# Optimization experiments

Hardware: AMD Instinct MI355X
Metric: run time of the kernel (lower is better)

Reference implementation:

```python
import jax, jax.numpy as jnp
import numpy as np

HEADS = 4
NEG_SLOPE = 0.2
LN_EPS = 1e-5


def _layernorm(h, g, b):
    mu = h.mean(-1, keepdims=True)
    var = ((h - mu) ** 2).mean(-1, keepdims=True)
    return (h - mu) / jnp.sqrt(var + LN_EPS) * g + b


def _forward(x, edge_attr, vnf_context,
             w_node, b_node, w_edge_emb, b_edge_emb,
             w_eproj, b_eproj, w_vnf, b_vnf,
             attn_w1, attn_b1, attn_w2, attn_b2, attn_w3, attn_b3,
             gat_w, gat_att_src, gat_att_dst, gat_we, gat_att_e, gat_b,
             ln_g, ln_b,
             venc_w1, venc_b1, venc_w2, venc_b2,
             lstm_wih, lstm_whh, lstm_bih, lstm_bhh,
             out_w1, out_b1, out_w2, out_b2, out_w3, out_b3,
             edge_index):
    N = x.shape[0]
    C = w_node.shape[1]  # hidden_dim = per-head out_channels
    L = gat_w.shape[0]
    src, dst = edge_index[0], edge_index[1]

    # embeddings
    xh = x @ w_node + b_node                        # [N, C]
    ea = edge_attr @ w_edge_emb + b_edge_emb        # [E, C]

    # EdgeAttentionLayer (vnf_context branch, no network_state)
    ef = ea @ w_eproj + b_eproj                     # [E, C]
    vemb = vnf_context @ w_vnf + b_vnf              # [C]
    comb = jnp.concatenate([ef, jnp.broadcast_to(vemb, ef.shape)], axis=-1)
    h1 = jax.nn.relu(comb @ attn_w1 + attn_b1)
    h2 = jax.nn.relu(h1 @ attn_w2 + attn_b2)
    edge_attention = jax.nn.sigmoid(h2 @ attn_w3 + attn_b3)[:, 0]   # [E]
    e_enh = ef * edge_attention[:, None]            # weighted edge features [E, C]

    # PathQualityAwareConv stack: GATConv(heads=4, concat=False, edge_dim=C)
    for l in range(L):
        xr = xh
        xs = (xh @ gat_w[l]).reshape(N, HEADS, C)               # [N, H, C]
        efeat = (e_enh @ gat_we[l]).reshape(-1, HEADS, C)        # [E, H, C]
        a = (jnp.einsum('ehc,hc->eh', xs[src], gat_att_src[l])
             + jnp.einsum('ehc,hc->eh', xs[dst], gat_att_dst[l])
             + jnp.einsum('ehc,hc->eh', efeat, gat_att_e[l]))
        a = jax.nn.leaky_relu(a, NEG_SLOPE)
        amax = jax.ops.segment_max(a, dst, num_segments=N)
        amax = jnp.where(jnp.isfinite(amax), amax, 0.0)
        ae = jnp.exp(a - amax[dst])
        denom = jax.ops.segment_sum(ae, dst, num_segments=N)
        alpha = ae / (denom[dst] + 1e-16)                        # [E, H]
        msg = xs[src] * alpha[:, :, None]                        # [E, H, C]
        agg = jax.ops.segment_sum(msg, dst, num_segments=N)      # [N, H, C]
        h = agg.mean(axis=1) + gat_b[l]                          # concat=False -> head mean
        h = _layernorm(h, ln_g[l], ln_b[l])
        xh = h + xr                                              # residual (same size)

    # vnf context encoder
    v = jax.nn.relu(vnf_context @ venc_w1 + venc_b1) @ venc_w2 + venc_b2  # [C]

    # Set2Set pooling, single graph, processing_steps=3, LSTM(2C -> C)
    hS = jnp.zeros((C,), xh.dtype)
    cS = jnp.zeros((C,), xh.dtype)
    q_star = jnp.zeros((2 * C,), xh.dtype)
    for _ in range(3):
        gates = lstm_wih @ q_star + lstm_bih + lstm_whh @ hS + lstm_bhh
        gi, gf, gg, go = jnp.split(gates, 4)
        cS = jax.nn.sigmoid(gf) * cS + jax.nn.sigmoid(gi) * jnp.tanh(gg)
        hS = jax.nn.sigmoid(go) * jnp.tanh(cS)
        q = hS
        a_sc = jax.nn.softmax(xh @ q)                            # [N]
        r = a_sc @ xh                                            # [C]
        q_star = jnp.concatenate([q, r])

    combined = jnp.concatenate([q_star, v])                      # [3C]
    o = jax.nn.relu(combined @ out_w1 + out_b1)
    o = jax.nn.relu(o @ out_w2 + out_b2)
    o = jax.nn.relu(o @ out_w3 + out_b3)
    return o[None, :]                                            # [1, output_dim]


def setup_inputs() -> dict:
    key = jax.random.key(0)
    ks = jax.random.split(key, 40)
    N, E, C, L = 50000, 200000, 128, 3
    H = HEADS
    rn = lambda k, s, sc=0.05: (jax.random.normal(k, s, jnp.float32) * sc)
    z = lambda *s: jnp.zeros(s, jnp.float32)
    return {
        'x': jax.random.normal(ks[0], (N, 8), jnp.float32),
        'edge_index': jax.random.randint(ks[1], (2, E), 0, N),
        'edge_attr': jax.random.uniform(ks[2], (E, 4), dtype=jnp.float32),
        'vnf_context': jax.random.normal(ks[3], (6,), jnp.float32),
        'w_node': rn(ks[4], (8, C)), 'b_node': z(C),
        'w_edge_emb': rn(ks[5], (4, C)), 'b_edge_emb': z(C),
        'w_eproj': rn(ks[6], (C, C)), 'b_eproj': z(C),
        'w_vnf': rn(ks[7], (6, C)), 'b_vnf': z(C),
        'attn_w1': rn(ks[8], (2 * C, C)), 'attn_b1': z(C),
        'attn_w2': rn(ks[9], (C, C // 2)), 'attn_b2': z(C // 2),
        'attn_w3': rn(ks[10], (C // 2, 1)), 'attn_b3': z(1),
        'gat_w': rn(ks[11], (L, C, H * C)),
        'gat_att_src': rn(ks[12], (L, H, C)),
        'gat_att_dst': rn(ks[13], (L, H, C)),
        'gat_we': rn(ks[14], (L, C, H * C)),
        'gat_att_e': rn(ks[15], (L, H, C)),
        'gat_b': z(L, C),
        'ln_g': jnp.ones((L, C), jnp.float32), 'ln_b': z(L, C),
        'venc_w1': rn(ks[16], (6, C)), 'venc_b1': z(C),
        'venc_w2': rn(ks[17], (C, C)), 'venc_b2': z(C),
        'lstm_wih': rn(ks[18], (4 * C, 2 * C)), 'lstm_whh': rn(ks[19], (4 * C, C)),
        'lstm_bih': z(4 * C), 'lstm_bhh': z(4 * C),
        'out_w1': rn(ks[20], (3 * C, C)), 'out_b1': z(C),
        'out_w2': rn(ks[21], (C, C // 2)), 'out_b2': z(C // 2),
        'out_w3': rn(ks[22], (C // 2, 256)), 'out_b3': z(256),
    }


def reference(x, edge_index, edge_attr, vnf_context,
              w_node, b_node, w_edge_emb, b_edge_emb,
              w_eproj, b_eproj, w_vnf, b_vnf,
              attn_w1, attn_b1, attn_w2, attn_b2, attn_w3, attn_b3,
              gat_w, gat_att_src, gat_att_dst, gat_we, gat_att_e, gat_b,
              ln_g, ln_b,
              venc_w1, venc_b1, venc_w2, venc_b2,
              lstm_wih, lstm_whh, lstm_bih, lstm_bhh,
              out_w1, out_b1, out_w2, out_b2, out_w3, out_b3):
    return _forward(x, edge_attr, vnf_context,
                    w_node, b_node, w_edge_emb, b_edge_emb,
                    w_eproj, b_eproj, w_vnf, b_vnf,
                    attn_w1, attn_b1, attn_w2, attn_b2, attn_w3, attn_b3,
                    gat_w, gat_att_src, gat_att_dst, gat_we, gat_att_e, gat_b,
                    ln_g, ln_b,
                    venc_w1, venc_b1, venc_w2, venc_b2,
                    lstm_wih, lstm_whh, lstm_bih, lstm_bhh,
                    out_w1, out_b1, out_w2, out_b2, out_w3, out_b3,
                    edge_index)
```

## Files before the change

### kernel.cpp

```cpp
#include <hip/hip_runtime.h>
#include <math.h>

#define CC 128
#define HH 4
#define LL 3
#define LNEPS 1e-5f

typedef unsigned int u32;
typedef unsigned short ushort;
typedef float f32x16 __attribute__((ext_vector_type(16)));
typedef __bf16 bf16x8 __attribute__((ext_vector_type(8)));
union Frag { uint4 q; bf16x8 b; };

__device__ __forceinline__ ushort bf16rne(float x){ u32 u=__float_as_uint(x); return (ushort)((u + 0x7FFF + ((u>>16)&1))>>16); }
__device__ __forceinline__ float bf2f(ushort h){ return __uint_as_float(((u32)h)<<16); }


__global__ void k_att_collapse(const float* __restrict__ W, const float* __restrict__ att, float* __restrict__ out){
  int idx = blockIdx.x*blockDim.x + threadIdx.x;
  if(idx >= LL*CC*HH) return;
  int h = idx % HH; int k = (idx/HH)%CC; int l = idx/(HH*CC);
  const float* w = W + ((size_t)(l*CC+k))*(HH*CC) + h*CC;
  const float* a = att + (size_t)(l*HH+h)*CC;
  float s=0.f;
  for(int c=0;c<CC;c++) s += w[c]*a[c];
  out[idx] = s;
}

__global__ void k_We(const float* __restrict__ w_ee, const float* __restrict__ w_ep, float* __restrict__ We){
  int idx = blockIdx.x*blockDim.x + threadIdx.x;
  if(idx >= 4*CC) return;
  int c = idx & (CC-1); int k = idx >> 7;
  float s=0.f;
  for(int m=0;m<CC;m++) s += w_ee[k*CC+m]*w_ep[m*CC+c];
  We[idx]=s;
}

__global__ void k_be_vemb(const float* __restrict__ b_ee, const float* __restrict__ w_ep, const float* __restrict__ b_ep,
                          const float* __restrict__ vnf, const float* __restrict__ w_vnf, const float* __restrict__ b_vnf,
                          float* __restrict__ be, float* __restrict__ vemb){
  int t = threadIdx.x;
  if(t<CC){
    float s=b_ep[t];
    for(int m=0;m<CC;m++) s += b_ee[m]*w_ep[m*CC+t];
    be[t]=s;
  } else if(t<2*CC){
    int c=t-CC;
    float s=b_vnf[c];
    for(int j=0;j<6;j++) s += vnf[j]*w_vnf[j*CC+c];
    vemb[c]=s;
  }
}

__global__ void k_h1eff(const float* __restrict__ We, const float* __restrict__ be, const float* __restrict__ vemb,
                        const float* __restrict__ w1, const float* __restrict__ b1,
                        float* __restrict__ Wh1, float* __restrict__ bh1){
  int idx = blockIdx.x*blockDim.x + threadIdx.x;
  if(idx < 4*CC){
    int c = idx & (CC-1); int k = idx>>7;
    float s=0.f;
    for(int m=0;m<CC;m++) s += We[k*CC+m]*w1[m*CC+c];
    Wh1[idx]=s;
  } else if(idx < 5*CC){
    int c = idx - 4*CC;
    float s=b1[c];
    for(int m=0;m<CC;m++) s += be[m]*w1[m*CC+c];
    for(int j=0;j<CC;j++) s += vemb[j]*w1[(CC+j)*CC+c];
    bh1[c]=s;
  }
}

__global__ void k_aelin(const float* __restrict__ We, const float* __restrict__ be, const float* __restrict__ wattE,
                        float* __restrict__ aelin, float* __restrict__ aebias){
  int t = threadIdx.x;
  if(t<48){
    int l=t>>4, k=(t>>2)&3, h=t&3;
    float s=0.f;
    for(int m=0;m<CC;m++) s += We[k*CC+m]*wattE[(size_t)(l*CC+m)*HH+h];
    aelin[t]=s;
  } else if(t<60){
    int i=t-48; int l=i>>2, h=i&3;
    float s=0.f;
    for(int m=0;m<CC;m++) s += be[m]*wattE[(size_t)(l*CC+m)*HH+h];
    aebias[i]=s;
  }
}

__global__ void k_wsplit(const float* __restrict__ gat_w, ushort* __restrict__ BT){
  int idx = blockIdx.x*blockDim.x + threadIdx.x;
  if(idx >= LL*512*CC) return;
  int l = idx >> 16;
  int r = idx & 65535;
  int hk = r >> 7;
  int c  = r & 127;
  int k = hk & 127, h = hk >> 7;
  float v = gat_w[((size_t)(l*CC + k))*(HH*CC) + h*CC + c] * 0.25f;
  ushort hi = bf16rne(v);
  ushort lo = bf16rne(v - bf2f(hi));
  size_t pos = (size_t)l*131072 + ((size_t)(c>>5)*64 + (hk>>3))*512 + (size_t)((c&31)*16 + (hk&7));
  BT[pos]=hi; BT[pos+8]=lo;
}

__global__ void k_vvec(const float* __restrict__ vnf, const float* __restrict__ w1, const float* __restrict__ b1,
                       const float* __restrict__ w2, const float* __restrict__ b2, float* __restrict__ v){
  __shared__ float hv[CC];
  int t=threadIdx.x;
  float s=b1[t];
  for(int j=0;j<6;j++) s += vnf[j]*w1[j*CC+t];
  hv[t]=fmaxf(s,0.f);
  __syncthreads();
  float o=b2[t];
  for(int j=0;j<CC;j++) o += hv[j]*w2[j*CC+t];
  v[t]=o;
}

__global__ void k_node_embed(const float* __restrict__ x, const float* __restrict__ w, const float* __restrict__ b,
                             float* __restrict__ xh, int N){
  int idx=blockIdx.x*blockDim.x+threadIdx.x;
  if(idx>=N*CC) return;
  int c=idx&(CC-1); int n=idx>>7;
  const float* xr = x+(size_t)n*8;
  float s=b[c];
  #pragma unroll
  for(int k=0;k<8;k++) s += xr[k]*w[k*CC+c];
  xh[idx]=s;
}

__global__ void k_count(const int* __restrict__ dst, int* __restrict__ counts, int E){
  int e=blockIdx.x*blockDim.x+threadIdx.x;
  if(e<E) atomicAdd(&counts[dst[e]],1);
}

__global__ __launch_bounds__(256) void k_scan_blk(const int* __restrict__ counts, int* __restrict__ offsets,
                                                  int* __restrict__ bsum, int N){
  __shared__ int sv[256];
  int t=threadIdx.x; int i=blockIdx.x*256+t;
  int v = (i<N)? counts[i] : 0;
  sv[t]=v;
  __syncthreads();
  for(int off=1;off<256;off<<=1){
    int add = (t>=off)? sv[t-off]:0;
    __syncthreads();
    sv[t]+=add;
    __syncthreads();
  }
  if(i<N) offsets[i]=sv[t]-v;
  if(t==255) bsum[blockIdx.x]=sv[255];
}

__global__ __launch_bounds__(1024) void k_scan_top(int* __restrict__ bsum, int nb){
  __shared__ int sv[1024];
  int t=threadIdx.x;
  int v = (t<nb)? bsum[t] : 0;
  sv[t]=v;
  __syncthreads();
  for(int off=1;off<1024;off<<=1){
    int add = (t>=off)? sv[t-off]:0;
    __syncthreads();
    sv[t]+=add;
    __syncthreads();
  }
  if(t<nb) bsum[t]=sv[t]-v;
}

__global__ void k_scan_add(int* __restrict__ offsets, const int* __restrict__ bsum, int N, int E){
  int i=blockIdx.x*blockDim.x+threadIdx.x;
  if(i<N) offsets[i]+=bsum[i>>8];
  if(i==0) offsets[N]=E;
}

__global__ void k_fill(const int* __restrict__ dst, const int* __restrict__ offsets, int* __restrict__ cursor,
                       int* __restrict__ elist, int E){
  int e=blockIdx.x*blockDim.x+threadIdx.x;
  if(e<E){ int d=dst[e]; int pos=atomicAdd(&cursor[d],1); elist[offsets[d]+pos]=e; }
}

__global__ __launch_bounds__(256) void k_edge_attn(
    const float* __restrict__ edge_attr,
    const float* __restrict__ Wh1, const float* __restrict__ bh1,
    const float* __restrict__ attn_w2, const float* __restrict__ attn_b2,
    const float* __restrict__ attn_w3, const float* __restrict__ attn_b3,
    const float* __restrict__ aelin, const float* __restrict__ aebias,
    float* __restrict__ a_e, int E)
{
  __shared__ float s_w2[64*64];
  __shared__ float s_h1t[64*64];
  __shared__ float s_eat[4*64];
  __shared__ float s_wh1t[CC*4];
  __shared__ float s_bh1[CC];
  __shared__ float s_b2[64];
  __shared__ float s_w3[64];
  __shared__ float s_lin[48];
  __shared__ float s_lbias[12];
  int t = threadIdx.x;
  for(int i=t;i<CC*4;i+=256){ int c=i>>2, k=i&3; s_wh1t[i]=Wh1[k*CC+c]; }
  if(t<CC) s_bh1[t]=bh1[t];
  else if(t<CC+64) s_b2[t-CC]=attn_b2[t-CC];
  else if(t<CC+128) s_w3[t-CC-64]=attn_w3[t-CC-64];
  if(t<48) s_lin[t]=aelin[t];
  else if(t<60) s_lbias[t-48]=aebias[t-48];
  float b3v = attn_b3[0];
  int e0 = blockIdx.x*64;
  if(t<64){
    int e=e0+t;
    float4 v = (e<E)? *(const float4*)&edge_attr[(size_t)e*4] : make_float4(0.f,0.f,0.f,0.f);
    s_eat[t]=v.x; s_eat[64+t]=v.y; s_eat[128+t]=v.z; s_eat[192+t]=v.w;
  }
  int eg=t>>4, og=t&15;
  float acc[4][4];
  #pragma unroll
  for(int i=0;i<4;i++){ acc[i][0]=0.f; acc[i][1]=0.f; acc[i][2]=0.f; acc[i][3]=0.f; }
  for(int half=0;half<2;half++){
    __syncthreads();
    for(int i=t;i<64*64;i+=256){
      int kl=i>>6, e=i&63, k=half*64+kl;
      float4 w = *(const float4*)&s_wh1t[k*4];
      float v = s_bh1[k] + s_eat[e]*w.x + s_eat[64+e]*w.y + s_eat[128+e]*w.z + s_eat[192+e]*w.w;
      s_h1t[i] = fmaxf(v,0.f);
    }
    for(int i=t;i<64*64;i+=256) s_w2[i] = attn_w2[half*4096 + i];
    __syncthreads();
    #pragma unroll 8
    for(int k=0;k<64;k++){
      float4 a = *(const float4*)&s_h1t[k*64 + eg*4];
      float4 b = *(const float4*)&s_w2[k*64 + og*4];
      acc[0][0]+=a.x*b.x; acc[0][1]+=a.x*b.y; acc[0][2]+=a.x*b.z; acc[0][3]+=a.x*b.w;
      acc[1][0]+=a.y*b.x; acc[1][1]+=a.y*b.y; acc[1][2]+=a.y*b.z; acc[1][3]+=a.y*b.w;
      acc[2][0]+=a.z*b.x; acc[2][1]+=a.z*b.y; acc[2][2]+=a.z*b.z; acc[2][3]+=a.z*b.w;
      acc[3][0]+=a.w*b.x; acc[3][1]+=a.w*b.y; acc[3][2]+=a.w*b.z; acc[3][3]+=a.w*b.w;
    }
  }
  float4 b2v = *(const float4*)&s_b2[og*4];
  float4 w3v = *(const float4*)&s_w3[og*4];
  float att[4];
  #pragma unroll
  for(int i=0;i<4;i++){
    float p = fmaxf(acc[i][0]+b2v.x,0.f)*w3v.x + fmaxf(acc[i][1]+b2v.y,0.f)*w3v.y
            + fmaxf(acc[i][2]+b2v.z,0.f)*w3v.z + fmaxf(acc[i][3]+b2v.w,0.f)*w3v.w;
    #pragma unroll
    for(int off=1;off<16;off<<=1) p += __shfl_xor(p,off);
    att[i] = 1.f/(1.f+expf(-(p+b3v)));
  }
  if(og<12){
    int l=og>>2, h=og&3;
    float w0=s_lin[l*16+h], w1=s_lin[l*16+4+h], w2x=s_lin[l*16+8+h], w3x=s_lin[l*16+12+h];
    float lb=s_lbias[l*4+h];
    #pragma unroll
    for(int i=0;i<4;i++){
      int el=eg*4+i; int e=e0+el;
      if(e<E){
        float v = s_eat[el]*w0 + s_eat[64+el]*w1 + s_eat[128+el]*w2x + s_eat[192+el]*w3x + lb;
        a_e[((size_t)l*E+e)*4+h] = att[i]*v;
      }
    }
  }
}

__global__ __launch_bounds__(256) void k_node_ad(const float* __restrict__ xh, const float* __restrict__ wS, const float* __restrict__ wD,
                          float* __restrict__ asrc, float* __restrict__ adst, int N){
  __shared__ float sx[32*129];
  __shared__ float sw[CC*8];
  int t = threadIdx.x;
  int n0 = blockIdx.x*32;
  for(int i=t;i<512;i+=256){ int k=i>>2, h=i&3; sw[k*8+h]=wS[i]; sw[k*8+4+h]=wD[i]; }
  int lim = (N-n0 < 32 ? N-n0 : 32)*128;
  for(int i=t;i<lim;i+=256){ int nl=i>>7, k=i&127; sx[nl*129+k] = xh[(size_t)n0*128 + i]; }
  __syncthreads();
  int node = t>>3, o = t&7;
  if(n0+node < N){
    const float* xr = sx + node*129;
    float s=0.f;
    #pragma unroll 8
    for(int k=0;k<CC;k++) s += xr[k]*sw[k*8+o];
    ((o<4)? asrc : adst)[(n0+node)*4 + (o&3)] = s;
  }
}

__global__ void k_alpha(const float* __restrict__ asrc, const float* __restrict__ adst,
                        const int* __restrict__ offsets, const int* __restrict__ elist,
                        const int* __restrict__ srcArr, float* __restrict__ ael, int N){
  int idx = blockIdx.x*blockDim.x + threadIdx.x;
  if(idx >= N*4) return;
  int n = idx>>2, h = idx&3;
  int beg = offsets[n], end = offsets[n+1];
  if(beg==end) return;
  float ad = adst[n*4+h];
  float m = -1e30f;
  for(int i=beg;i<end;i++){
    int e = elist[i];
    float a = asrc[srcArr[e]*4+h] + ad + ael[e*4+h];
    a = (a>0.f)? a : 0.2f*a;
    m = fmaxf(m,a);
  }
  float s=0.f;
  for(int i=beg;i<end;i++){
    int e = elist[i];
    float a = asrc[srcArr[e]*4+h] + ad + ael[e*4+h];
    a = (a>0.f)? a : 0.2f*a;
    float ex = expf(a-m);
    s += ex;
    ael[e*4+h] = ex;
  }
  float inv = 1.f/(s+1e-16f);
  for(int i=beg;i<end;i++){
    int e = elist[i];
    ael[e*4+h] *= inv;
  }
}

__global__ __launch_bounds__(256) void k_aggregate(
    const float* __restrict__ xh, const int* __restrict__ srcArr,
    const float* __restrict__ alpha, const int* __restrict__ offsets, const int* __restrict__ elist,
    ushort* __restrict__ AB, int N)
{
  __shared__ __align__(16) ushort sAB[4][64][16];
  int wave = threadIdx.x>>6, lane = threadIdx.x&63;
  int n = blockIdx.x*4+wave;
  float2 ac[4];
  #pragma unroll
  for(int h=0;h<4;h++){ ac[h].x=0.f; ac[h].y=0.f; }
  if(n<N){
    int beg = offsets[n], end = offsets[n+1];
    const float4* al4 = (const float4*)alpha;
    for(int i=beg;i<end;i++){
      int e = elist[i];
      int sr = srcArr[e];
      float4 a = al4[e];
      float2 x = *(const float2*)&xh[(size_t)sr*CC + lane*2];
      ac[0].x += a.x*x.x; ac[0].y += a.x*x.y;
      ac[1].x += a.y*x.x; ac[1].y += a.y*x.y;
      ac[2].x += a.z*x.x; ac[2].y += a.z*x.y;
      ac[3].x += a.w*x.x; ac[3].y += a.w*x.y;
    }
  }
  #pragma unroll
  for(int h=0;h<4;h++){
    ushort h0 = bf16rne(ac[h].x), h1 = bf16rne(ac[h].y);
    u32 hi = (u32)h0 | ((u32)h1<<16);
    u32 lo = (u32)bf16rne(ac[h].x - bf2f(h0)) | ((u32)bf16rne(ac[h].y - bf2f(h1))<<16);
    int hk = h*CC + lane*2;
    int st = hk>>3, off = hk&7;
    *(u32*)&sAB[wave][st][off]   = hi;
    *(u32*)&sAB[wave][st][off+8] = lo;
  }
  __syncthreads();
  int n0 = blockIdx.x*4;
  size_t tilebase = ((size_t)(n0>>5))*32768 + (size_t)((n0&31)*16);
  for(int i=threadIdx.x; i<512; i+=256){
    int st = i>>3, p = i&7;
    uint4 v = *(const uint4*)&sAB[p>>1][st][(p&1)*8];
    *(uint4*)&AB[tilebase + (size_t)st*512 + (size_t)p*8] = v;
  }
}

__global__ __launch_bounds__(128) void k_gemm_ln_mfma(
    const ushort* __restrict__ AB, const ushort* __restrict__ BT,
    const float* __restrict__ bias, const float* __restrict__ lng, const float* __restrict__ lnb,
    float* __restrict__ xh, int N)
{
  int tid = threadIdx.x;
  int w = tid>>6, lane = tid&63;
  int rlane = lane&31, khalf = lane>>5;
  int rb = blockIdx.x*2 + w;
  f32x16 acc[4];
  #pragma unroll
  for(int t=0;t<4;t++)
    #pragma unroll
    for(int j=0;j<16;j++) acc[t][j]=0.f;

  const size_t laneoff = (size_t)(rlane*16);
  for(int ks=0; ks<32; ++ks){
    int kq = ks*2 + khalf;
    size_t base = ((size_t)(rb*64 + kq))*512 + laneoff;
    Frag ah, al;
    ah.q = *(const uint4*)(AB + base);
    al.q = *(const uint4*)(AB + base + 8);
    #pragma unroll
    for(int t=0;t<4;t++){
      size_t bb = ((size_t)(t*64 + kq))*512 + laneoff;
      Frag bh, bl;
      bh.q = *(const uint4*)(BT + bb);
      bl.q = *(const uint4*)(BT + bb + 8);
      acc[t] = __builtin_amdgcn_mfma_f32_32x32x16_bf16(ah.b, bh.b, acc[t], 0,0,0);
      acc[t] = __builtin_amdgcn_mfma_f32_32x32x16_bf16(ah.b, bl.b, acc[t], 0,0,0);
      acc[t] = __builtin_amdgcn_mfma_f32_32x32x16_bf16(al.b, bh.b, acc[t], 0,0,0);
    }
  }
  float bias4[4], g4[4], eb4[4];
  #pragma unroll
  for(int t=0;t<4;t++){ int c=t*32+rlane; bias4[t]=bias[c]; g4[t]=lng[c]; eb4[t]=lnb[c]; }
  #pragma unroll
  for(int reg=0; reg<16; ++reg){
    int rloc = (reg&3) + 8*(reg>>2) + 4*khalf;
    int grow = rb*32 + rloc;
    float x0=acc[0][reg]+bias4[0];
    float x1=acc[1][reg]+bias4[1];
    float x2=acc[2][reg]+bias4[2];
    float x3=acc[3][reg]+bias4[3];
    float s = x0+x1+x2+x3;
    #pragma unroll
    for(int off=1; off<32; off<<=1) s += __shfl_xor(s, off);
    float mu = s*(1.f/CC);
    x0-=mu; x1-=mu; x2-=mu; x3-=mu;
    float q = x0*x0+x1*x1+x2*x2+x3*x3;
    #pragma unroll
    for(int off=1; off<32; off<<=1) q += __shfl_xor(q, off);
    float inv = rsqrtf(q*(1.f/CC)+LNEPS);
    if(grow < N){
      size_t gi = (size_t)grow*CC + rlane;
      xh[gi+ 0]  = x0*inv*g4[0] + eb4[0] + xh[gi+ 0];
      xh[gi+32]  = x1*inv*g4[1] + eb4[1] + xh[gi+32];
      xh[gi+64]  = x2*inv*g4[2] + eb4[2] + xh[gi+64];
      xh[gi+96]  = x3*inv*g4[3] + eb4[3] + xh[gi+96];
    }
  }
}

__global__ __launch_bounds__(512) void k_lstm(const float* __restrict__ wih, const float* __restrict__ whh,
                    const float* __restrict__ bih, const float* __restrict__ bhh,
                    const float* __restrict__ qstar, float* __restrict__ hS, float* __restrict__ cS){
  __shared__ float sq[2*CC];
  __shared__ float sh[CC];
  __shared__ float sg[4*CC];
  int t=threadIdx.x;
  if(t<2*CC) sq[t]=qstar[t];
  else if(t<3*CC) sh[t-2*CC]=hS[t-2*CC];
  __syncthreads();
  float a=bih[t]+bhh[t];
  const float* wr = wih + (size_t)t*2*CC;
  for(int j=0;j<2*CC;j++) a += wr[j]*sq[j];
  const float* hr = whh + (size_t)t*CC;
  for(int j=0;j<CC;j++) a += hr[j]*sh[j];
  sg[t]=a;
  __syncthreads();
  if(t<CC){
    float gi=sg[t], gf=sg[CC+t], gg=sg[2*CC+t], go=sg[3*CC+t];
    float c = 1.f/(1.f+expf(-gf))*cS[t] + 1.f/(1.f+expf(-gi))*tanhf(gg);
    float h = 1.f/(1.f+expf(-go))*tanhf(c);
    cS[t]=c; hS[t]=h;
  }
}

__global__ __launch_bounds__(256) void k_s2s1(const float* __restrict__ xh, const float* __restrict__ q,
                                              float* __restrict__ pm, float* __restrict__ ps,
                                              float* __restrict__ pr, int N){
  int t=threadIdx.x, wave=t>>6, lane=t&63;
  float q0=q[lane], q1=q[lane+64];
  float m=-1e30f, s=0.f, r0=0.f, r1=0.f;
  for(int n=blockIdx.x*4+wave; n<N; n+=gridDim.x*4){
    const float* xr = xh+(size_t)n*CC;
    float x0 = xr[lane], x1 = xr[lane+64];
    float v = x0*q0 + x1*q1;
    #pragma unroll
    for(int o=32;o>=1;o>>=1) v += __shfl_xor(v,o);
    float nm = fmaxf(m,v);
    float f = expf(m-nm), g = expf(v-nm);
    s = s*f + g; r0 = r0*f + g*x0; r1 = r1*f + g*x1;
    m = nm;
  }
  __shared__ float sm[4], ss[4], sr[4][128];
  if(lane==0){ sm[wave]=m; ss[wave]=s; }
  sr[wave][lane]=r0; sr[wave][lane+64]=r1;
  __syncthreads();
  if(t<128){
    float M = fmaxf(fmaxf(sm[0],sm[1]),fmaxf(sm[2],sm[3]));
    float e0=expf(sm[0]-M), e1=expf(sm[1]-M), e2=expf(sm[2]-M), e3=expf(sm[3]-M);
    pr[(size_t)blockIdx.x*128+t] = sr[0][t]*e0 + sr[1][t]*e1 + sr[2][t]*e2 + sr[3][t]*e3;
    if(t==0){ pm[blockIdx.x]=M; ps[blockIdx.x]= ss[0]*e0+ss[1]*e1+ss[2]*e2+ss[3]*e3; }
  }
}

__global__ __launch_bounds__(1024) void k_s2s2(const float* __restrict__ pm, const float* __restrict__ ps,
                                               const float* __restrict__ pr, const float* __restrict__ hS,
                                               float* __restrict__ qstar, int NB){
  __shared__ float sM[256];
  __shared__ float sw[256];
  __shared__ float sS[256];
  __shared__ float srs[8][128];
  int t = threadIdx.x;
  if(t<256) sM[t] = (t<NB)? pm[t] : -1e30f;
  __syncthreads();
  for(int off=128; off>=1; off>>=1){
    if(t<off) sM[t] = fmaxf(sM[t], sM[t+off]);
    __syncthreads();
  }
  float M = sM[0];
  if(t<256){
    float w = (t<NB)? expf(pm[t]-M) : 0.f;
    sw[t] = w;
    sS[t] = (t<NB)? ps[t]*w : 0.f;
  }
  __syncthreads();
  for(int off=128; off>=1; off>>=1){
    if(t<off) sS[t] += sS[t+off];
    __syncthreads();
  }
  float ssum = sS[0];
  int g = t>>7, col = t&127;
  float rs = 0.f;
  for(int b=g; b<NB; b+=8) rs += pr[(size_t)b*128+col]*sw[b];
  srs[g][col] = rs;
  __syncthreads();
  if(t<128){
    float r = srs[0][t]+srs[1][t]+srs[2][t]+srs[3][t]+srs[4][t]+srs[5][t]+srs[6][t]+srs[7][t];
    qstar[t]    = hS[t];
    qstar[CC+t] = r/ssum;
  }
}

__global__ __launch_bounds__(256) void k_out(
  const float* __restrict__ qstar, const float* __restrict__ vvec,
  const float* __restrict__ w1, const float* __restrict__ b1,
  const float* __restrict__ w2, const float* __restrict__ b2,
  const float* __restrict__ w3, const float* __restrict__ b3, float* __restrict__ out)
{
  __shared__ float comb[3*CC];
  __shared__ float o1[CC];
  __shared__ float o2[64];
  int t=threadIdx.x;
  if(t<2*CC) comb[t]=qstar[t];
  if(t<CC) comb[2*CC+t]=vvec[t];
  __syncthreads();
  if(t<CC){
    float a=b1[t];
    for(int j=0;j<3*CC;j++) a += comb[j]*w1[j*CC+t];
    o1[t]=fmaxf(a,0.f);
  }
  __syncthreads();
  if(t<64){
    float a=b2[t];
    for(int j=0;j<CC;j++) a += o1[j]*w2[j*64+t];
    o2[t]=fmaxf(a,0.f);
  }
  __syncthreads();
  {
    float a=b3[t];
    for(int j=0;j<64;j++) a += o2[j]*w3[j*256+t];
    out[t]=fmaxf(a,0.f);
  }
}

extern "C" void kernel_launch(void* const* d_in, const int* in_sizes, int n_in,
                              void* d_out, int out_size, void* d_ws, size_t ws_size,
                              hipStream_t stream){
  (void)n_in; (void)out_size; (void)ws_size;
  const float* x        = (const float*)d_in[0];
  const int*   eidx     = (const int*)  d_in[1];
  const float* edge_attr= (const float*)d_in[2];
  const float* vnf      = (const float*)d_in[3];
  const float* w_node   = (const float*)d_in[4];
  const float* b_node   = (const float*)d_in[5];
  const float* w_ee     = (const float*)d_in[6];
  const float* b_ee     = (const float*)d_in[7];
  const float* w_ep     = (const float*)d_in[8];
  const float* b_ep     = (const float*)d_in[9];
  const float* w_vnf    = (const float*)d_in[10];
  const float* b_vnf    = (const float*)d_in[11];
  const float* attn_w1  = (const float*)d_in[12];
  const float* attn_b1  = (const float*)d_in[13];
  const float* attn_w2  = (const float*)d_in[14];
  const float* attn_b2  = (const float*)d_in[15];
  const float* attn_w3  = (const float*)d_in[16];
  const float* attn_b3  = (const float*)d_in[17];
  const float* gat_w    = (const float*)d_in[18];
  const float* att_src  = (const float*)d_in[19];
  const float* att_dst  = (const float*)d_in[20];
  const float* gat_we   = (const float*)d_in[21];
  const float* att_e    = (const float*)d_in[22];
  const float* gat_b    = (const float*)d_in[23];
  const float* ln_g     = (const float*)d_in[24];
  const float* ln_b     = (const float*)d_in[25];
  const float* venc_w1  = (const float*)d_in[26];
  const float* venc_b1  = (const float*)d_in[27];
  const float* venc_w2  = (const float*)d_in[28];
  const float* venc_b2  = (const float*)d_in[29];
  const float* lstm_wih = (const float*)d_in[30];
  const float* lstm_whh = (const float*)d_in[31];
  const float* lstm_bih = (const float*)d_in[32];
  const float* lstm_bhh = (const float*)d_in[33];
  const float* out_w1   = (const float*)d_in[34];
  const float* out_b1   = (const float*)d_in[35];
  const float* out_w2   = (const float*)d_in[36];
  const float* out_b2   = (const float*)d_in[37];
  const float* out_w3   = (const float*)d_in[38];
  const float* out_b3   = (const float*)d_in[39];

  const int N = in_sizes[0]/8;
  const int E = in_sizes[1]/2;
  const int* srcA = eidx;
  const int* dstA = eidx + E;

  const int Npad = ((N+127)/128)*128;
  const size_t asize = (size_t)Npad*1024;
  const int nb = (N+255)/256;
  const int S2SB = 256;

  char* wp = (char*)d_ws;
  auto alloc = [&](size_t bytes)->void*{ void* p=(void*)wp; wp += (bytes+255)&~(size_t)255; return p; };
  float* xh    = (float*)alloc((size_t)N*CC*4);
  ushort* AB   = (ushort*)alloc(asize*2);
  ushort* BT   = (ushort*)alloc((size_t)LL*131072*2);
  float* a_e   = (float*)alloc((size_t)LL*E*HH*4);
  float* asrc  = (float*)alloc((size_t)N*HH*4);
  float* adst  = (float*)alloc((size_t)N*HH*4);
  int* counts  = (int*)alloc((size_t)N*4);
  int* offsets = (int*)alloc((size_t)(N+1)*4);
  int* cursor  = (int*)alloc((size_t)N*4);
  int* elist   = (int*)alloc((size_t)E*4);
  int* bsum    = (int*)alloc((size_t)nb*4);
  float* wattS = (float*)alloc((size_t)LL*CC*HH*4);
  float* wattD = (float*)alloc((size_t)LL*CC*HH*4);
  float* wattE = (float*)alloc((size_t)LL*CC*HH*4);
  float* We    = (float*)alloc(4*CC*4);
  float* be    = (float*)alloc(CC*4);
  float* vemb  = (float*)alloc(CC*4);
  float* Wh1   = (float*)alloc(4*CC*4);
  float* bh1   = (float*)alloc(CC*4);
  float* aelin = (float*)alloc(48*4);
  float* aebias= (float*)alloc(12*4);
  float* vvec  = (float*)alloc(CC*4);
  float* lbuf  = (float*)alloc(4*CC*4);
  float* hS=lbuf; float* cS=lbuf+CC; float* qstar=lbuf+2*CC;
  float* pm    = (float*)alloc((size_t)S2SB*4);
  float* ps    = (float*)alloc((size_t)S2SB*4);
  float* pr    = (float*)alloc((size_t)S2SB*128*4);

  k_att_collapse<<<6,256,0,stream>>>(gat_w, att_src, wattS);
  k_att_collapse<<<6,256,0,stream>>>(gat_w, att_dst, wattD);
  k_att_collapse<<<6,256,0,stream>>>(gat_we, att_e, wattE);
  k_We<<<2,256,0,stream>>>(w_ee, w_ep, We);
  k_be_vemb<<<1,256,0,stream>>>(b_ee, w_ep, b_ep, vnf, w_vnf, b_vnf, be, vemb);
  k_h1eff<<<3,256,0,stream>>>(We, be, vemb, attn_w1, attn_b1, Wh1, bh1);
  k_aelin<<<1,64,0,stream>>>(We, be, wattE, aelin, aebias);
  k_wsplit<<<(LL*512*CC+255)/256,256,0,stream>>>(gat_w, BT);
  k_vvec<<<1,CC,0,stream>>>(vnf, venc_w1, venc_b1, venc_w2, venc_b2, vvec);
  k_node_embed<<<(N*CC+255)/256,256,0,stream>>>(x, w_node, b_node, xh, N);

  hipMemsetAsync(counts, 0, (size_t)N*4, stream);
  k_count<<<(E+255)/256,256,0,stream>>>(dstA, counts, E);
  k_scan_blk<<<nb,256,0,stream>>>(counts, offsets, bsum, N);
  k_scan_top<<<1,1024,0,stream>>>(bsum, nb);
  k_scan_add<<<nb,256,0,stream>>>(offsets, bsum, N, E);
  hipMemsetAsync(cursor, 0, (size_t)N*4, stream);
  k_fill<<<(E+255)/256,256,0,stream>>>(dstA, offsets, cursor, elist, E);

  k_edge_attn<<<(E+63)/64,256,0,stream>>>(edge_attr, Wh1, bh1, attn_w2, attn_b2, attn_w3, attn_b3, aelin, aebias, a_e, E);

  for(int l=0;l<LL;l++){
    float* ael = a_e + (size_t)l*E*HH;
    k_node_ad<<<(N+31)/32,256,0,stream>>>(xh, wattS+(size_t)l*CC*HH, wattD+(size_t)l*CC*HH, asrc, adst, N);
    k_alpha<<<(N*4+255)/256,256,0,stream>>>(asrc, adst, offsets, elist, srcA, ael, N);
    k_aggregate<<<(N+3)/4,256,0,stream>>>(xh, srcA, ael, offsets, elist, AB, N);
    k_gemm_ln_mfma<<<Npad/64,128,0,stream>>>(AB, BT+(size_t)l*131072,
                                             gat_b+(size_t)l*CC, ln_g+(size_t)l*CC, ln_b+(size_t)l*CC, xh, N);
  }

  hipMemsetAsync(lbuf, 0, 4*CC*4, stream);
  for(int it=0; it<3; ++it){
    k_lstm<<<1,512,0,stream>>>(lstm_wih, lstm_whh, lstm_bih, lstm_bhh, qstar, hS, cS);
    k_s2s1<<<S2SB,256,0,stream>>>(xh, hS, pm, ps, pr, N);
    k_s2s2<<<1,1024,0,stream>>>(pm, ps, pr, hS, qstar, S2SB);
  }

  k_out<<<1,256,0,stream>>>(qstar, vvec, out_w1, out_b1, out_w2, out_b2, out_w3, out_b3, (float*)d_out);
}
```

Baseline: 790.8 us.

## Compute edge-attention MLP hidden layer with split-bf16 MFMA

Replaces the FP32 scalar 64x128x64 GEMM in the edge attention kernel with MFMA 32x32x16 bf16 instructions, using a hi/lo bf16 split (three products) to keep near-FP32 accuracy. The attn_w2 weights are pre-split and laid out in a fragment-friendly order by a new setup kernel, and the h1 activations are written to shared memory directly in fragment layout. Block size drops to 128 threads and shared memory use shrinks. This is meant to cut ALU time in the per-edge MLP, at the cost of an extra small kernel launch and reduced-precision products.

New measurement: 779.9 us (median of 2 runs). Within noise of the previous version (-1.4%).

```diff
diff --git a/kernel.cpp b/kernel.cpp
--- a/kernel.cpp
+++ b/kernel.cpp
@@ -101,6 +101,17 @@
   BT[pos]=hi; BT[pos+8]=lo;
 }
 
+__global__ void k_w2split(const float* __restrict__ w2, ushort* __restrict__ W2T){
+  int idx = blockIdx.x*blockDim.x + threadIdx.x;
+  if(idx >= 128*64) return;
+  int k = idx>>6, o = idx&63;
+  float v = w2[idx];
+  ushort hi = bf16rne(v);
+  ushort lo = bf16rne(v - bf2f(hi));
+  size_t pos = ((size_t)(o>>5)*16 + (k>>3))*512 + (size_t)((o&31)*16 + (k&7));
+  W2T[pos]=hi; W2T[pos+8]=lo;
+}
+
 __global__ void k_vvec(const float* __restrict__ vnf, const float* __restrict__ w1, const float* __restrict__ b1,
                        const float* __restrict__ w2, const float* __restrict__ b2, float* __restrict__ v){
   __shared__ float hv[CC];
@@ -175,82 +186,95 @@
   if(e<E){ int d=dst[e]; int pos=atomicAdd(&cursor[d],1); elist[offsets[d]+pos]=e; }
 }
 
-__global__ __launch_bounds__(256) void k_edge_attn(
+__global__ __launch_bounds__(128) void k_edge_attn(
     const float* __restrict__ edge_attr,
     const float* __restrict__ Wh1, const float* __restrict__ bh1,
-    const float* __restrict__ attn_w2, const float* __restrict__ attn_b2,
+    const ushort* __restrict__ W2T, const float* __restrict__ attn_b2,
     const float* __restrict__ attn_w3, const float* __restrict__ attn_b3,
     const float* __restrict__ aelin, const float* __restrict__ aebias,
     float* __restrict__ a_e, int E)
 {
-  __shared__ float s_w2[64*64];
-  __shared__ float s_h1t[64*64];
-  __shared__ float s_eat[4*64];
-  __shared__ float s_wh1t[CC*4];
-  __shared__ float s_bh1[CC];
-  __shared__ float s_b2[64];
-  __shared__ float s_w3[64];
-  __shared__ float s_lin[48];
-  __shared__ float s_lbias[12];
+  __shared__ __align__(16) ushort h1f[2][16][32][16];
+  __shared__ float s_wh1[640];
+  __shared__ float s_ea[64][4];
+  __shared__ float s_att[64];
   int t = threadIdx.x;
-  for(int i=t;i<CC*4;i+=256){ int c=i>>2, k=i&3; s_wh1t[i]=Wh1[k*CC+c]; }
-  if(t<CC) s_bh1[t]=bh1[t];
-  else if(t<CC+64) s_b2[t-CC]=attn_b2[t-CC];
-  else if(t<CC+128) s_w3[t-CC-64]=attn_w3[t-CC-64];
-  if(t<48) s_lin[t]=aelin[t];
-  else if(t<60) s_lbias[t-48]=aebias[t-48];
-  float b3v = attn_b3[0];
   int e0 = blockIdx.x*64;
+  for(int i=t;i<640;i+=128) s_wh1[i] = (i<512)? Wh1[i] : bh1[i-512];
   if(t<64){
     int e=e0+t;
     float4 v = (e<E)? *(const float4*)&edge_attr[(size_t)e*4] : make_float4(0.f,0.f,0.f,0.f);
-    s_eat[t]=v.x; s_eat[64+t]=v.y; s_eat[128+t]=v.z; s_eat[192+t]=v.w;
-  }
-  int eg=t>>4, og=t&15;
-  float acc[4][4];
-  #pragma unroll
-  for(int i=0;i<4;i++){ acc[i][0]=0.f; acc[i][1]=0.f; acc[i][2]=0.f; acc[i][3]=0.f; }
-  for(int half=0;half<2;half++){
-    __syncthreads();
-    for(int i=t;i<64*64;i+=256){
-      int kl=i>>6, e=i&63, k=half*64+kl;
-      float4 w = *(const float4*)&s_wh1t[k*4];
-      float v = s_bh1[k] + s_eat[e]*w.x + s_eat[64+e]*w.y + s_eat[128+e]*w.z + s_eat[192+e]*w.w;
-      s_h1t[i] = fmaxf(v,0.f);
+    s_ea[t][0]=v.x; s_ea[t][1]=v.y; s_ea[t][2]=v.z; s_ea[t][3]=v.w;
+  }
+  __syncthreads();
+  for(int c=t; c<1024; c+=128){
+    int e = c&63, kc = c>>6;
+    int et = e>>5, row = e&31;
+    float ea0=s_ea[e][0], ea1=s_ea[e][1], ea2=s_ea[e][2], ea3=s_ea[e][3];
+    ushort hibuf[8], lobuf[8];
+    #pragma unroll
+    for(int j=0;j<8;j++){
+      int k = kc*8+j;
+      float v = s_wh1[512+k] + ea0*s_wh1[k] + ea1*s_wh1[128+k] + ea2*s_wh1[256+k] + ea3*s_wh1[384+k];
+      v = fmaxf(v, 0.f);
+      ushort hi = bf16rne(v);
+      hibuf[j]=hi; lobuf[j]=bf16rne(v - bf2f(hi));
     }
-    for(int i=t;i<64*64;i+=256) s_w2[i] = attn_w2[half*4096 + i];
-    __syncthreads();
-    #pragma unroll 8
-    for(int k=0;k<64;k++){
-      float4 a = *(const float4*)&s_h1t[k*64 + eg*4];
-      float4 b = *(const float4*)&s_w2[k*64 + og*4];
-      acc[0][0]+=a.x*b.x; acc[0][1]+=a.x*b.y; acc[0][2]+=a.x*b.z; acc[0][3]+=a.x*b.w;
-      acc[1][0]+=a.y*b.x; acc[1][1]+=a.y*b.y; acc[1][2]+=a.y*b.z; acc[1][3]+=a.y*b.w;
-      acc[2][0]+=a.z*b.x; acc[2][1]+=a.z*b.y; acc[2][2]+=a.z*b.z; acc[2][3]+=a.z*b.w;
-      acc[3][0]+=a.w*b.x; acc[3][1]+=a.w*b.y; acc[3][2]+=a.w*b.z; acc[3][3]+=a.w*b.w;
+    *(uint4*)&h1f[et][kc][row][0] = *(const uint4*)hibuf;
+    *(uint4*)&h1f[et][kc][row][8] = *(const uint4*)lobuf;
+  }
+  __syncthreads();
+  int wave=t>>6, lane=t&63;
+  int rlane = lane&31, khalf = lane>>5;
+  int et = wave;
+  f32x16 acc[2];
+  #pragma unroll
+  for(int o=0;o<2;o++)
+    #pragma unroll
+    for(int j=0;j<16;j++) acc[o][j]=0.f;
+  for(int ks=0; ks<8; ++ks){
+    int kq = ks*2 + khalf;
+    Frag ah, al;
+    ah.q = *(const uint4*)&h1f[et][kq][rlane][0];
+    al.q = *(const uint4*)&h1f[et][kq][rlane][8];
+    #pragma unroll
+    for(int o=0;o<2;o++){
+      size_t bb = ((size_t)(o*16 + kq))*512 + (size_t)(rlane*16);
+      Frag bh, bl;
+      bh.q = *(const uint4*)(W2T + bb);
+      bl.q = *(const uint4*)(W2T + bb + 8);
+      acc[o] = __builtin_amdgcn_mfma_f32_32x32x16_bf16(ah.b, bh.b, acc[o], 0,0,0);
+      acc[o] = __builtin_amdgcn_mfma_f32_32x32x16_bf16(ah.b, bl.b, acc[o], 0,0,0);
+      acc[o] = __builtin_amdgcn_mfma_f32_32x32x16_bf16(al.b, bh.b, acc[o], 0,0,0);
     }
   }
-  float4 b2v = *(const float4*)&s_b2[og*4];
-  float4 w3v = *(const float4*)&s_w3[og*4];
-  float att[4];
-  #pragma unroll
-  for(int i=0;i<4;i++){
-    float p = fmaxf(acc[i][0]+b2v.x,0.f)*w3v.x + fmaxf(acc[i][1]+b2v.y,0.f)*w3v.y
-            + fmaxf(acc[i][2]+b2v.z,0.f)*w3v.z + fmaxf(acc[i][3]+b2v.w,0.f)*w3v.w;
-    #pragma unroll
-    for(int off=1;off<16;off<<=1) p += __shfl_xor(p,off);
-    att[i] = 1.f/(1.f+expf(-(p+b3v)));
-  }
-  if(og<12){
-    int l=og>>2, h=og&3;
-    float w0=s_lin[l*16+h], w1=s_lin[l*16+4+h], w2x=s_lin[l*16+8+h], w3x=s_lin[l*16+12+h];
-    float lb=s_lbias[l*4+h];
-    #pragma unroll
-    for(int i=0;i<4;i++){
-      int el=eg*4+i; int e=e0+el;
-      if(e<E){
-        float v = s_eat[el]*w0 + s_eat[64+el]*w1 + s_eat[128+el]*w2x + s_eat[192+el]*w3x + lb;
-        a_e[((size_t)l*E+e)*4+h] = att[i]*v;
+  float b2c0 = attn_b2[rlane], b2c1 = attn_b2[rlane+32];
+  float w3c0 = attn_w3[rlane], w3c1 = attn_w3[rlane+32];
+  float b3v = attn_b3[0];
+  #pragma unroll
+  for(int reg=0; reg<16; ++reg){
+    float val = fmaxf(acc[0][reg]+b2c0,0.f)*w3c0 + fmaxf(acc[1][reg]+b2c1,0.f)*w3c1;
+    #pragma unroll
+    for(int off=1; off<32; off<<=1) val += __shfl_xor(val, off);
+    int rloc = (reg&3) + 8*(reg>>2) + 4*khalf;
+    if(rlane==0) s_att[et*32 + rloc] = 1.f/(1.f+expf(-(val + b3v)));
+  }
+  __syncthreads();
+  if(t<64){
+    int e = e0+t;
+    if(e<E){
+      float att = s_att[t];
+      float ea0=s_ea[t][0], ea1=s_ea[t][1], ea2=s_ea[t][2], ea3=s_ea[t][3];
+      #pragma unroll
+      for(int l=0;l<LL;l++){
+        float4 v;
+        float* out=(float*)&v;
+        #pragma unroll
+        for(int h=0;h<4;h++){
+          out[h] = att*(ea0*aelin[(l*4+0)*4+h] + ea1*aelin[(l*4+1)*4+h]
+                      + ea2*aelin[(l*4+2)*4+h] + ea3*aelin[(l*4+3)*4+h] + aebias[l*4+h]);
+        }
+        *(float4*)&a_e[((size_t)l*E+e)*4] = v;
       }
     }
   }
@@ -600,6 +624,7 @@
   float* xh    = (float*)alloc((size_t)N*CC*4);
   ushort* AB   = (ushort*)alloc(asize*2);
   ushort* BT   = (ushort*)alloc((size_t)LL*131072*2);
+  ushort* W2T  = (ushort*)alloc((size_t)16384*2);
   float* a_e   = (float*)alloc((size_t)LL*E*HH*4);
   float* asrc  = (float*)alloc((size_t)N*HH*4);
   float* adst  = (float*)alloc((size_t)N*HH*4);
@@ -633,6 +658,7 @@
   k_h1eff<<<3,256,0,stream>>>(We, be, vemb, attn_w1, attn_b1, Wh1, bh1);
   k_aelin<<<1,64,0,stream>>>(We, be, wattE, aelin, aebias);
   k_wsplit<<<(LL*512*CC+255)/256,256,0,stream>>>(gat_w, BT);
+  k_w2split<<<(128*64+255)/256,256,0,stream>>>(attn_w2, W2T);
   k_vvec<<<1,CC,0,stream>>>(vnf, venc_w1, venc_b1, venc_w2, venc_b2, vvec);
   k_node_embed<<<(N*CC+255)/256,256,0,stream>>>(x, w_node, b_node, xh, N);
 
@@ -644,7 +670,7 @@
   hipMemsetAsync(cursor, 0, (size_t)N*4, stream);
   k_fill<<<(E+255)/256,256,0,stream>>>(dstA, offsets, cursor, elist, E);
 
-  k_edge_attn<<<(E+63)/64,256,0,stream>>>(edge_attr, Wh1, bh1, attn_w2, attn_b2, attn_w3, attn_b3, aelin, aebias, a_e, E);
+  k_edge_attn<<<(E+63)/64,128,0,stream>>>(edge_attr, Wh1, bh1, W2T, attn_b2, attn_w3, attn_b3, aelin, aebias, a_e, E);
 
   for(int l=0;l<LL;l++){
     float* ael = a_e + (size_t)l*E*HH;
```
